# Optimization experiments

Measured on AMD Instinct MI355X. Metric: run time of the kernel, lower is better.

Reference implementation:

```python
import jax, jax.numpy as jnp
import numpy as np

N_NODES = 100000
N_EDGES = 1600000
NFEAT = 256
NHID = 128


def _l2_normalize(v, eps=1e-12):
    return v / (jnp.linalg.norm(v) + eps)


def setup_inputs() -> dict:
    key = jax.random.key(0)
    k1, k2, k3, k4 = jax.random.split(key, 4)
    x = jax.random.normal(k1, (N_NODES, NFEAT), dtype=jnp.float32)
    edge_index = jax.random.randint(k2, (2, N_EDGES), 0, N_NODES, dtype=jnp.int64)
    # GCNConv weight (glorot-ish scale), spectral-normalized at forward time
    W = jax.random.normal(k3, (NFEAT, NHID), dtype=jnp.float32) * 0.05
    bias = jnp.zeros((NHID,), dtype=jnp.float32)
    prelu_a = jnp.full((1,), 0.25, dtype=jnp.float32)  # nn.PReLU default slope
    u = _l2_normalize(jax.random.normal(k4, (NFEAT,), dtype=jnp.float32))
    return {"x": x, "edge_index": edge_index, "W": W, "bias": bias,
            "prelu_a": prelu_a, "u": u}


def reference(x, edge_index, W, bias, prelu_a, u):
    # --- spectral_norm: one power iteration (torch default n_power_iterations=1) ---
    v = _l2_normalize(W.T @ u)          # [NHID]
    u2 = _l2_normalize(W @ v)           # [NFEAT]
    sigma = u2 @ (W @ v)
    W_sn = W / sigma

    # --- GCNConv: linear transform, add self-loops, sym-normalize, scatter-add ---
    xw = x @ W_sn                       # [N, NHID]
    n = x.shape[0]
    loops = jnp.arange(n, dtype=edge_index.dtype)
    row = jnp.concatenate([edge_index[0], loops])  # sources
    col = jnp.concatenate([edge_index[1], loops])  # targets
    ones = jnp.ones(row.shape[0], dtype=x.dtype)
    deg = jax.ops.segment_sum(ones, col, num_segments=n)
    dinv = jnp.where(deg > 0, deg ** -0.5, 0.0)
    norm = dinv[row] * dinv[col]        # [E+N]
    msgs = norm[:, None] * xw[row]      # gather at sources
    out = jax.ops.segment_sum(msgs, col, num_segments=n) + bias

    # --- PReLU ---
    return jnp.where(out > 0, out, prelu_a * out)
```

## Files before the change

### kernel.cpp

```cpp
#include <hip/hip_runtime.h>

#define NFEAT 256
#define NHID  128

#define NBK   391
#define EPB   4096
#define NBLK  391
#define SEGW  4608

typedef __bf16 bf16x8 __attribute__((ext_vector_type(8)));
typedef __bf16 bf16x4 __attribute__((ext_vector_type(4)));
typedef float  f32x4  __attribute__((ext_vector_type(4)));

__global__ __launch_bounds__(256) void sigma_kernel(const float* __restrict__ W,
                                                    const float* __restrict__ u,
                                                    float* __restrict__ scal,
                                                    int* __restrict__ bucket_fill) {
    __shared__ float v[NHID];
    __shared__ float red[256];
    int tid = threadIdx.x;

    if (tid < NBK) bucket_fill[tid] = 0;
    if (tid + 256 < NBK) bucket_fill[tid + 256] = 0;

    float t = 0.f;
    if (tid < NHID) {
        for (int i = 0; i < NFEAT; ++i) t += W[i * NHID + tid] * u[i];
    }
    red[tid] = (tid < NHID) ? t * t : 0.f;
    __syncthreads();
    for (int s = 128; s > 0; s >>= 1) {
        if (tid < s) red[tid] += red[tid + s];
        __syncthreads();
    }
    float nv = sqrtf(red[0]);
    float inv_nv = 1.f / (nv + 1e-12f);
    __syncthreads();
    if (tid < NHID) v[tid] = t * inv_nv;
    __syncthreads();

    float wv = 0.f;
    for (int j = 0; j < NHID; ++j) wv += W[tid * NHID + j] * v[j];
    red[tid] = wv * wv;
    __syncthreads();
    for (int s = 128; s > 0; s >>= 1) {
        if (tid < s) red[tid] += red[tid + s];
        __syncthreads();
    }
    if (tid == 0) {
        float n2  = red[0];
        float nwv = sqrtf(n2);
        float sigma = n2 / (nwv + 1e-12f);
        scal[0] = 1.f / sigma;
    }
}

__global__ __launch_bounds__(256) void wt_kernel(const float* __restrict__ W,
                                                 const float* __restrict__ scal,
                                                 __bf16* __restrict__ WT) {
    int idx = blockIdx.x * 256 + threadIdx.x;
    int c = idx >> 8;
    int r = idx & 255;
    WT[c * NFEAT + r] = (__bf16)(W[r * NHID + c] * scal[0]);
}

__global__ __launch_bounds__(256) void fused_kernel(const float* __restrict__ x,
                                                    const __bf16* __restrict__ WT,
                                                    __bf16* __restrict__ xwb,
                                                    const int* __restrict__ erow,
                                                    const int* __restrict__ ecol,
                                                    int* __restrict__ bucket_fill,
                                                    unsigned int* __restrict__ rbuf,
                                                    int nn, int E, int ngemm) {
    __shared__ __attribute__((aligned(16))) char sbuf[32768];

    int tid  = threadIdx.x;

    if ((int)blockIdx.x < ngemm) {
        float (*xs)[64][64] = (float (*)[64][64])sbuf;

        int lane = tid & 63;
        int w    = tid >> 6;
        int rfrag = lane & 15;
        int kg    = lane >> 4;
        int row0 = blockIdx.x * 64;

        int p16  = lane & 15;
        int rsub = lane >> 4;

        int crow0 = (w & 1) * 32 + rfrag;
        int col0  = (w >> 1) * 64;
        int r0 = row0 + crow0;
        int r1 = r0 + 16;
        const __bf16* wb = WT + (size_t)(col0 + rfrag) * NFEAT + kg * 8;
        int cr7 = crow0 & 7;

        f32x4 acc0[4] = {};
        f32x4 acc1[4] = {};

        auto STAGE = [&](int buf, int c) {
#pragma unroll
            for (int j = 0; j < 4; ++j) {
                int rloc = w * 16 + j * 4 + rsub;
                int grow = row0 + rloc;
                if (grow >= nn) grow = nn - 1;
                const float* src = x + (size_t)grow * NFEAT + c * 64 + ((p16 ^ (grow & 7)) << 2);
                __builtin_amdgcn_global_load_lds(
                    (const __attribute__((address_space(1))) void*)src,
                    (__attribute__((address_space(3))) void*)&xs[buf][w * 16 + j * 4][0],
                    16, 0, 0);
            }
        };

        bf16x8 Bf[2][2][4];
        auto BLOAD = [&](int bbuf, int c) {
#pragma unroll
            for (int ks = 0; ks < 2; ++ks)
#pragma unroll
                for (int nt = 0; nt < 4; ++nt)
                    Bf[bbuf][ks][nt] = *(const bf16x8*)(wb + (size_t)nt * 16 * NFEAT + c * 64 + ks * 32);
        };

        auto MFMA_CHUNK = [&](int buf, int bbuf) {
#pragma unroll
            for (int ks = 0; ks < 2; ++ks) {
                int sA = kg * 2 + ks * 8;
                float4 a0lo = *(const float4*)&xs[buf][crow0][((sA) ^ cr7) * 4];
                float4 a0hi = *(const float4*)&xs[buf][crow0][((sA + 1) ^ cr7) * 4];
                float4 a1lo = *(const float4*)&xs[buf][crow0 + 16][((sA) ^ cr7) * 4];
                float4 a1hi = *(const float4*)&xs[buf][crow0 + 16][((sA + 1) ^ cr7) * 4];
                bf16x8 af0, af1;
                af0[0] = (__bf16)a0lo.x; af0[1] = (__bf16)a0lo.y;
                af0[2] = (__bf16)a0lo.z; af0[3] = (__bf16)a0lo.w;
                af0[4] = (__bf16)a0hi.x; af0[5] = (__bf16)a0hi.y;
                af0[6] = (__bf16)a0hi.z; af0[7] = (__bf16)a0hi.w;
                af1[0] = (__bf16)a1lo.x; af1[1] = (__bf16)a1lo.y;
                af1[2] = (__bf16)a1lo.z; af1[3] = (__bf16)a1lo.w;
                af1[4] = (__bf16)a1hi.x; af1[5] = (__bf16)a1hi.y;
                af1[6] = (__bf16)a1hi.z; af1[7] = (__bf16)a1hi.w;
#pragma unroll
                for (int nt = 0; nt < 4; ++nt) {
                    acc0[nt] = __builtin_amdgcn_mfma_f32_16x16x32_bf16(Bf[bbuf][ks][nt], af0, acc0[nt], 0, 0, 0);
                    acc1[nt] = __builtin_amdgcn_mfma_f32_16x16x32_bf16(Bf[bbuf][ks][nt], af1, acc1[nt], 0, 0, 0);
                }
            }
        };

#define DRAIN_BAR() do { \
            asm volatile("s_waitcnt vmcnt(0)" ::: "memory"); \
            __builtin_amdgcn_s_barrier(); } while (0)

        STAGE(0, 0);
        BLOAD(0, 0);
        DRAIN_BAR();

        BLOAD(1, 1);
        STAGE(1, 1);
        __builtin_amdgcn_sched_barrier(0);
        MFMA_CHUNK(0, 0);
        DRAIN_BAR();

        BLOAD(0, 2);
        STAGE(0, 2);
        __builtin_amdgcn_sched_barrier(0);
        MFMA_CHUNK(1, 1);
        DRAIN_BAR();

        BLOAD(1, 3);
        STAGE(1, 3);
        __builtin_amdgcn_sched_barrier(0);
        MFMA_CHUNK(0, 0);
        DRAIN_BAR();

        MFMA_CHUNK(1, 1);
#undef DRAIN_BAR

        if (r0 < nn) {
            __bf16* orow = xwb + (size_t)r0 * NHID + col0 + kg * 4;
#pragma unroll
            for (int nt = 0; nt < 4; ++nt) {
                bf16x4 v;
                v[0] = (__bf16)acc0[nt][0];
                v[1] = (__bf16)acc0[nt][1];
                v[2] = (__bf16)acc0[nt][2];
                v[3] = (__bf16)acc0[nt][3];
                *(bf16x4*)&orow[nt * 16] = v;
            }
        }
        if (r1 < nn) {
            __bf16* orow = xwb + (size_t)r1 * NHID + col0 + kg * 4;
#pragma unroll
            for (int nt = 0; nt < 4; ++nt) {
                bf16x4 v;
                v[0] = (__bf16)acc1[nt][0];
                v[1] = (__bf16)acc1[nt][1];
                v[2] = (__bf16)acc1[nt][2];
                v[3] = (__bf16)acc1[nt][3];
                *(bf16x4*)&orow[nt * 16] = v;
            }
        }
        return;
    }

    unsigned int*   rec   = (unsigned int*)sbuf;
    unsigned short* bkk   = (unsigned short*)(sbuf + 16384);
    int*            hist  = (int*)(sbuf + 24576);
    int*            lbase = (int*)(sbuf + 24576 + 1564);
    int*            lfill = (int*)(sbuf + 24576 + 3128);
    int*            gb    = (int*)(sbuf + 24576 + 4692);

    int b = blockIdx.x - ngemm;
    for (int k = tid; k < NBK; k += 256) { hist[k] = 0; lfill[k] = 0; }
    __syncthreads();

    int e0 = b * EPB;
    unsigned int rv[16];
    int kv[16];
#pragma unroll
    for (int j = 0; j < 16; ++j) {
        int idx = e0 + j * 256 + tid;
        if (idx < E) {
            int c = ecol[idx];
            int s = erow[idx];
            int k = c >> 8;
            kv[j] = k;
            rv[j] = ((unsigned int)(c & 255) << 24) | (unsigned int)s;
            atomicAdd(&hist[k], 1);
        } else kv[j] = -1;
    }
    __syncthreads();

    if (tid < 64) {
        int carry = 0;
        for (int c0 = 0; c0 < NBK; c0 += 64) {
            int i = c0 + tid;
            int vv = (i < NBK) ? hist[i] : 0;
            int orig = vv;
#pragma unroll
            for (int d = 1; d < 64; d <<= 1) {
                int t = __shfl_up(vv, (unsigned)d, 64);
                if (tid >= d) vv += t;
            }
            if (i < NBK) lbase[i] = carry + vv - orig;
            carry += __shfl(vv, 63, 64);
        }
    }
    __syncthreads();

    if (tid < NBK) gb[tid] = tid * SEGW + atomicAdd(&bucket_fill[tid], hist[tid]);
    if (tid + 256 < NBK) gb[tid + 256] = (tid + 256) * SEGW
                                       + atomicAdd(&bucket_fill[tid + 256], hist[tid + 256]);
    __syncthreads();

#pragma unroll
    for (int j = 0; j < 16; ++j) {
        if (kv[j] >= 0) {
            int p = lbase[kv[j]] + atomicAdd(&lfill[kv[j]], 1);
            rec[p] = rv[j];
            bkk[p] = (unsigned short)kv[j];
        }
    }
    __syncthreads();

    int nval = E - e0;
    if (nval > EPB) nval = EPB;
    for (int p = tid; p < nval; p += 256) {
        int k = bkk[p];
        rbuf[gb[k] + (p - lbase[k])] = rec[p];
    }
}

__global__ __launch_bounds__(256) void fine_kernel(const unsigned int* __restrict__ rbuf,
                                                   const int* __restrict__ bucket_fill,
                                                   int* __restrict__ base_g,
                                                   int* __restrict__ cnt_g,
                                                   float* __restrict__ dinv,
                                                   int* __restrict__ ebuf, int n) {
    __shared__ int cnt[256], lb[256], lf[256], sc[256];
    int tid = threadIdx.x, k = blockIdx.x;
    int seg0 = k * SEGW, seg1 = seg0 + bucket_fill[k];
    cnt[tid] = 0;
    lf[tid] = 0;
    __syncthreads();
    for (int j = seg0 + tid; j < seg1; j += 256)
        atomicAdd(&cnt[rbuf[j] >> 24], 1);
    __syncthreads();
    int cv = cnt[tid];
    sc[tid] = cv;
    __syncthreads();
    int val = cv;
    for (int off = 1; off < 256; off <<= 1) {
        int t = (tid >= off) ? sc[tid - off] : 0;
        __syncthreads();
        val += t;
        sc[tid] = val;
        __syncthreads();
    }
    lb[tid] = val - cv;
    __syncthreads();
    int node = k * 256 + tid;
    if (node < n) {
        base_g[node] = seg0 + lb[tid];
        cnt_g[node] = cv;
        dinv[node] = rsqrtf((float)cv + 1.f);
    }
    for (int j = seg0 + tid; j < seg1; j += 256) {
        unsigned int r = rbuf[j];
        int dl = r >> 24;
        int p = seg0 + lb[dl] + atomicAdd(&lf[dl], 1);
        ebuf[p] = (int)(r & 0xFFFFFFu);
    }
}

__global__ __launch_bounds__(256) void gather_kernel(const uint4* __restrict__ xb4,
                                                     const int* __restrict__ base,
                                                     const int* __restrict__ cnt,
                                                     const int* __restrict__ ebuf,
                                                     const float* __restrict__ dinv,
                                                     const float* __restrict__ bias,
                                                     const float* __restrict__ pa,
                                                     float* __restrict__ out, int n) {
    int tid = threadIdx.x;
    int sub = tid & 15;
    int node = (blockIdx.x * 256 + tid) >> 4;
    if (node >= n) return;

    int b = base[node];
    int deg = cnt[node];
    float dn = dinv[node];

    uint4 s0 = xb4[(size_t)node * 16 + sub];
    float a0 = dn * __uint_as_float(s0.x << 16);
    float a1 = dn * __uint_as_float(s0.x & 0xffff0000u);
    float a2 = dn * __uint_as_float(s0.y << 16);
    float a3 = dn * __uint_as_float(s0.y & 0xffff0000u);
    float a4 = dn * __uint_as_float(s0.z << 16);
    float a5 = dn * __uint_as_float(s0.z & 0xffff0000u);
    float a6 = dn * __uint_as_float(s0.w << 16);
    float a7 = dn * __uint_as_float(s0.w & 0xffff0000u);

    int k = 0;
    for (; k + 4 <= deg; k += 4) {
        int r0 = ebuf[b + k + 0];
        int r1 = ebuf[b + k + 1];
        int r2 = ebuf[b + k + 2];
        int r3 = ebuf[b + k + 3];
        float d0 = dinv[r0], d1 = dinv[r1], d2 = dinv[r2], d3 = dinv[r3];
        uint4 v0 = xb4[(size_t)r0 * 16 + sub];
        uint4 v1 = xb4[(size_t)r1 * 16 + sub];
        uint4 v2 = xb4[(size_t)r2 * 16 + sub];
        uint4 v3 = xb4[(size_t)r3 * 16 + sub];
        a0 += d0 * __uint_as_float(v0.x << 16) + d1 * __uint_as_float(v1.x << 16)
            + d2 * __uint_as_float(v2.x << 16) + d3 * __uint_as_float(v3.x << 16);
        a1 += d0 * __uint_as_float(v0.x & 0xffff0000u) + d1 * __uint_as_float(v1.x & 0xffff0000u)
            + d2 * __uint_as_float(v2.x & 0xffff0000u) + d3 * __uint_as_float(v3.x & 0xffff0000u);
        a2 += d0 * __uint_as_float(v0.y << 16) + d1 * __uint_as_float(v1.y << 16)
            + d2 * __uint_as_float(v2.y << 16) + d3 * __uint_as_float(v3.y << 16);
        a3 += d0 * __uint_as_float(v0.y & 0xffff0000u) + d1 * __uint_as_float(v1.y & 0xffff0000u)
            + d2 * __uint_as_float(v2.y & 0xffff0000u) + d3 * __uint_as_float(v3.y & 0xffff0000u);
        a4 += d0 * __uint_as_float(v0.z << 16) + d1 * __uint_as_float(v1.z << 16)
            + d2 * __uint_as_float(v2.z << 16) + d3 * __uint_as_float(v3.z << 16);
        a5 += d0 * __uint_as_float(v0.z & 0xffff0000u) + d1 * __uint_as_float(v1.z & 0xffff0000u)
            + d2 * __uint_as_float(v2.z & 0xffff0000u) + d3 * __uint_as_float(v3.z & 0xffff0000u);
        a6 += d0 * __uint_as_float(v0.w << 16) + d1 * __uint_as_float(v1.w << 16)
            + d2 * __uint_as_float(v2.w << 16) + d3 * __uint_as_float(v3.w << 16);
        a7 += d0 * __uint_as_float(v0.w & 0xffff0000u) + d1 * __uint_as_float(v1.w & 0xffff0000u)
            + d2 * __uint_as_float(v2.w & 0xffff0000u) + d3 * __uint_as_float(v3.w & 0xffff0000u);
    }
    for (; k < deg; ++k) {
        int r = ebuf[b + k];
        float d = dinv[r];
        uint4 v = xb4[(size_t)r * 16 + sub];
        a0 += d * __uint_as_float(v.x << 16);
        a1 += d * __uint_as_float(v.x & 0xffff0000u);
        a2 += d * __uint_as_float(v.y << 16);
        a3 += d * __uint_as_float(v.y & 0xffff0000u);
        a4 += d * __uint_as_float(v.z << 16);
        a5 += d * __uint_as_float(v.z & 0xffff0000u);
        a6 += d * __uint_as_float(v.w << 16);
        a7 += d * __uint_as_float(v.w & 0xffff0000u);
    }

    float alpha = pa[0];
    const float4* bb4 = (const float4*)bias;
    float4 b0 = bb4[sub * 2], b1 = bb4[sub * 2 + 1];
    float o0 = dn * a0 + b0.x;
    float o1 = dn * a1 + b0.y;
    float o2 = dn * a2 + b0.z;
    float o3 = dn * a3 + b0.w;
    float o4 = dn * a4 + b1.x;
    float o5 = dn * a5 + b1.y;
    float o6 = dn * a6 + b1.z;
    float o7 = dn * a7 + b1.w;
    o0 = o0 > 0.f ? o0 : alpha * o0;
    o1 = o1 > 0.f ? o1 : alpha * o1;
    o2 = o2 > 0.f ? o2 : alpha * o2;
    o3 = o3 > 0.f ? o3 : alpha * o3;
    o4 = o4 > 0.f ? o4 : alpha * o4;
    o5 = o5 > 0.f ? o5 : alpha * o5;
    o6 = o6 > 0.f ? o6 : alpha * o6;
    o7 = o7 > 0.f ? o7 : alpha * o7;
    float4* orow = (float4*)out + (size_t)node * 32 + sub * 2;
    orow[0] = make_float4(o0, o1, o2, o3);
    orow[1] = make_float4(o4, o5, o6, o7);
}

extern "C" void kernel_launch(void* const* d_in, const int* in_sizes, int n_in,
                              void* d_out, int out_size, void* d_ws, size_t ws_size,
                              hipStream_t stream) {
    const float* x    = (const float*)d_in[0];
    const int*   ei   = (const int*)d_in[1];
    const float* W    = (const float*)d_in[2];
    const float* bias = (const float*)d_in[3];
    const float* pa   = (const float*)d_in[4];
    const float* u    = (const float*)d_in[5];

    int n = in_sizes[0] / NFEAT;
    int e = in_sizes[1] / 2;
    const int* erow = ei;
    const int* ecol = ei + e;

    float* out = (float*)d_out;
    char* ws = (char*)d_ws;
    float*        scal   = (float*)(ws);
    int*          bfill  = (int*)  (ws + 0x0002000);
    __bf16*       WT     = (__bf16*)(ws + 0x0010000);
    int*          base_g = (int*)  (ws + 0x0100000);
    int*          cnt_g  = (int*)  (ws + 0x0200000);
    float*        dinv   = (float*)(ws + 0x0300000);
    unsigned int* rbuf   = (unsigned int*)(ws + 0x0500000);
    int*          ebuf   = (int*)  (ws + 0x0C00000);
    __bf16*       xwb    = (__bf16*)(ws + 0x1300000);

    int ngemm = (n + 63) / 64;

    sigma_kernel<<<1, 256, 0, stream>>>(W, u, scal, bfill);
    wt_kernel<<<(NFEAT * NHID) / 256, 256, 0, stream>>>(W, scal, WT);

    fused_kernel<<<ngemm + NBLK, 256, 0, stream>>>(x, WT, xwb, erow, ecol,
                                                   bfill, rbuf, n, e, ngemm);

    fine_kernel<<<NBK, 256, 0, stream>>>(rbuf, bfill, base_g, cnt_g, dinv, ebuf, n);

    long long gunits = (long long)n * 16;
    gather_kernel<<<(int)((gunits + 255) / 256), 256, 0, stream>>>(
        (const uint4*)xwb, base_g, cnt_g, ebuf, dinv, bias, pa, out, n);
}
```

Measured before the change: 146.2 us.

## Split gather feature columns across blocks and pack per-node metadata

The gather kernel now gives each block one 16-column slice of the output for 32 nodes. Consecutive blocks share the same nodes but cover different column slices, so each block's random reads of neighbor rows touch a smaller part of xw, which may improve cache locality. Each thread loads 4 bytes per neighbor instead of 16, which gives more threads and more in-flight loads but narrower accesses, and edge indices and dinv are re-read 8 times. Per-node base, count and dinv are packed into one int4 so they come from a single load.

```diff
diff --git a/kernel.cpp b/kernel.cpp
--- a/kernel.cpp
+++ b/kernel.cpp
@@ -272,8 +272,7 @@
 
 __global__ __launch_bounds__(256) void fine_kernel(const unsigned int* __restrict__ rbuf,
                                                    const int* __restrict__ bucket_fill,
-                                                   int* __restrict__ base_g,
-                                                   int* __restrict__ cnt_g,
+                                                   int4* __restrict__ meta,
                                                    float* __restrict__ dinv,
                                                    int* __restrict__ ebuf, int n) {
     __shared__ int cnt[256], lb[256], lf[256], sc[256];
@@ -300,9 +299,14 @@
     __syncthreads();
     int node = k * 256 + tid;
     if (node < n) {
-        base_g[node] = seg0 + lb[tid];
-        cnt_g[node] = cv;
-        dinv[node] = rsqrtf((float)cv + 1.f);
+        float dv = rsqrtf((float)cv + 1.f);
+        int4 m;
+        m.x = seg0 + lb[tid];
+        m.y = cv;
+        m.z = __float_as_int(dv);
+        m.w = 0;
+        meta[node] = m;
+        dinv[node] = dv;
     }
     for (int j = seg0 + tid; j < seg1; j += 256) {
         unsigned int r = rbuf[j];
@@ -312,32 +316,28 @@
     }
 }
 
-__global__ __launch_bounds__(256) void gather_kernel(const uint4* __restrict__ xb4,
-                                                     const int* __restrict__ base,
-                                                     const int* __restrict__ cnt,
+__global__ __launch_bounds__(256) void gather_kernel(const unsigned int* __restrict__ xbd,
+                                                     const int4* __restrict__ meta,
                                                      const int* __restrict__ ebuf,
                                                      const float* __restrict__ dinv,
                                                      const float* __restrict__ bias,
                                                      const float* __restrict__ pa,
                                                      float* __restrict__ out, int n) {
     int tid = threadIdx.x;
-    int sub = tid & 15;
-    int node = (blockIdx.x * 256 + tid) >> 4;
+    int l = tid & 7;
+    int s = blockIdx.x & 7;
+    int node = (blockIdx.x >> 3) * 32 + (tid >> 3);
     if (node >= n) return;
 
-    int b = base[node];
-    int deg = cnt[node];
-    float dn = dinv[node];
-
-    uint4 s0 = xb4[(size_t)node * 16 + sub];
-    float a0 = dn * __uint_as_float(s0.x << 16);
-    float a1 = dn * __uint_as_float(s0.x & 0xffff0000u);
-    float a2 = dn * __uint_as_float(s0.y << 16);
-    float a3 = dn * __uint_as_float(s0.y & 0xffff0000u);
-    float a4 = dn * __uint_as_float(s0.z << 16);
-    float a5 = dn * __uint_as_float(s0.z & 0xffff0000u);
-    float a6 = dn * __uint_as_float(s0.w << 16);
-    float a7 = dn * __uint_as_float(s0.w & 0xffff0000u);
+    int4 m = meta[node];
+    int b = m.x, deg = m.y;
+    float dn = __int_as_float(m.z);
+    int co = s * 8 + l;
+    const unsigned int* xc = xbd + co;
+
+    unsigned int v = xc[(size_t)node * 64];
+    float a0 = dn * __uint_as_float(v << 16);
+    float a1 = dn * __uint_as_float(v & 0xffff0000u);
 
     int k = 0;
     for (; k + 4 <= deg; k += 4) {
@@ -346,63 +346,30 @@
         int r2 = ebuf[b + k + 2];
         int r3 = ebuf[b + k + 3];
         float d0 = dinv[r0], d1 = dinv[r1], d2 = dinv[r2], d3 = dinv[r3];
-        uint4 v0 = xb4[(size_t)r0 * 16 + sub];
-        uint4 v1 = xb4[(size_t)r1 * 16 + sub];
-        uint4 v2 = xb4[(size_t)r2 * 16 + sub];
-        uint4 v3 = xb4[(size_t)r3 * 16 + sub];
-        a0 += d0 * __uint_as_float(v0.x << 16) + d1 * __uint_as_float(v1.x << 16)
-            + d2 * __uint_as_float(v2.x << 16) + d3 * __uint_as_float(v3.x << 16);
-        a1 += d0 * __uint_as_float(v0.x & 0xffff0000u) + d1 * __uint_as_float(v1.x & 0xffff0000u)
-            + d2 * __uint_as_float(v2.x & 0xffff0000u) + d3 * __uint_as_float(v3.x & 0xffff0000u);
-        a2 += d0 * __uint_as_float(v0.y << 16) + d1 * __uint_as_float(v1.y << 16)
-            + d2 * __uint_as_float(v2.y << 16) + d3 * __uint_as_float(v3.y << 16);
-        a3 += d0 * __uint_as_float(v0.y & 0xffff0000u) + d1 * __uint_as_float(v1.y & 0xffff0000u)
-            + d2 * __uint_as_float(v2.y & 0xffff0000u) + d3 * __uint_as_float(v3.y & 0xffff0000u);
-        a4 += d0 * __uint_as_float(v0.z << 16) + d1 * __uint_as_float(v1.z << 16)
-            + d2 * __uint_as_float(v2.z << 16) + d3 * __uint_as_float(v3.z << 16);
-        a5 += d0 * __uint_as_float(v0.z & 0xffff0000u) + d1 * __uint_as_float(v1.z & 0xffff0000u)
-            + d2 * __uint_as_float(v2.z & 0xffff0000u) + d3 * __uint_as_float(v3.z & 0xffff0000u);
-        a6 += d0 * __uint_as_float(v0.w << 16) + d1 * __uint_as_float(v1.w << 16)
-            + d2 * __uint_as_float(v2.w << 16) + d3 * __uint_as_float(v3.w << 16);
-        a7 += d0 * __uint_as_float(v0.w & 0xffff0000u) + d1 * __uint_as_float(v1.w & 0xffff0000u)
-            + d2 * __uint_as_float(v2.w & 0xffff0000u) + d3 * __uint_as_float(v3.w & 0xffff0000u);
+        unsigned int v0 = xc[(size_t)r0 * 64];
+        unsigned int v1 = xc[(size_t)r1 * 64];
+        unsigned int v2 = xc[(size_t)r2 * 64];
+        unsigned int v3 = xc[(size_t)r3 * 64];
+        a0 += d0 * __uint_as_float(v0 << 16) + d1 * __uint_as_float(v1 << 16)
+            + d2 * __uint_as_float(v2 << 16) + d3 * __uint_as_float(v3 << 16);
+        a1 += d0 * __uint_as_float(v0 & 0xffff0000u) + d1 * __uint_as_float(v1 & 0xffff0000u)
+            + d2 * __uint_as_float(v2 & 0xffff0000u) + d3 * __uint_as_float(v3 & 0xffff0000u);
     }
     for (; k < deg; ++k) {
         int r = ebuf[b + k];
         float d = dinv[r];
-        uint4 v = xb4[(size_t)r * 16 + sub];
-        a0 += d * __uint_as_float(v.x << 16);
-        a1 += d * __uint_as_float(v.x & 0xffff0000u);
-        a2 += d * __uint_as_float(v.y << 16);
-        a3 += d * __uint_as_float(v.y & 0xffff0000u);
-        a4 += d * __uint_as_float(v.z << 16);
-        a5 += d * __uint_as_float(v.z & 0xffff0000u);
-        a6 += d * __uint_as_float(v.w << 16);
-        a7 += d * __uint_as_float(v.w & 0xffff0000u);
+        unsigned int vv = xc[(size_t)r * 64];
+        a0 += d * __uint_as_float(vv << 16);
+        a1 += d * __uint_as_float(vv & 0xffff0000u);
     }
 
     float alpha = pa[0];
-    const float4* bb4 = (const float4*)bias;
-    float4 b0 = bb4[sub * 2], b1 = bb4[sub * 2 + 1];
-    float o0 = dn * a0 + b0.x;
-    float o1 = dn * a1 + b0.y;
-    float o2 = dn * a2 + b0.z;
-    float o3 = dn * a3 + b0.w;
-    float o4 = dn * a4 + b1.x;
-    float o5 = dn * a5 + b1.y;
-    float o6 = dn * a6 + b1.z;
-    float o7 = dn * a7 + b1.w;
+    float2 bb = ((const float2*)bias)[co];
+    float o0 = dn * a0 + bb.x;
+    float o1 = dn * a1 + bb.y;
     o0 = o0 > 0.f ? o0 : alpha * o0;
     o1 = o1 > 0.f ? o1 : alpha * o1;
-    o2 = o2 > 0.f ? o2 : alpha * o2;
-    o3 = o3 > 0.f ? o3 : alpha * o3;
-    o4 = o4 > 0.f ? o4 : alpha * o4;
-    o5 = o5 > 0.f ? o5 : alpha * o5;
-    o6 = o6 > 0.f ? o6 : alpha * o6;
-    o7 = o7 > 0.f ? o7 : alpha * o7;
-    float4* orow = (float4*)out + (size_t)node * 32 + sub * 2;
-    orow[0] = make_float4(o0, o1, o2, o3);
-    orow[1] = make_float4(o4, o5, o6, o7);
+    ((float2*)out)[(size_t)node * 64 + co] = make_float2(o0, o1);
 }
 
 extern "C" void kernel_launch(void* const* d_in, const int* in_sizes, int n_in,
@@ -425,12 +392,11 @@
     float*        scal   = (float*)(ws);
     int*          bfill  = (int*)  (ws + 0x0002000);
     __bf16*       WT     = (__bf16*)(ws + 0x0010000);
-    int*          base_g = (int*)  (ws + 0x0100000);
-    int*          cnt_g  = (int*)  (ws + 0x0200000);
-    float*        dinv   = (float*)(ws + 0x0300000);
-    unsigned int* rbuf   = (unsigned int*)(ws + 0x0500000);
-    int*          ebuf   = (int*)  (ws + 0x0C00000);
-    __bf16*       xwb    = (__bf16*)(ws + 0x1300000);
+    float*        dinv   = (float*)(ws + 0x0100000);
+    int4*         meta   = (int4*) (ws + 0x0200000);
+    unsigned int* rbuf   = (unsigned int*)(ws + 0x0400000);
+    int*          ebuf   = (int*)  (ws + 0x0B00000);
+    __bf16*       xwb    = (__bf16*)(ws + 0x1200000);
 
     int ngemm = (n + 63) / 64;
 
@@ -440,9 +406,9 @@
     fused_kernel<<<ngemm + NBLK, 256, 0, stream>>>(x, WT, xwb, erow, ecol,
                                                    bfill, rbuf, n, e, ngemm);
 
-    fine_kernel<<<NBK, 256, 0, stream>>>(rbuf, bfill, base_g, cnt_g, dinv, ebuf, n);
-
-    long long gunits = (long long)n * 16;
-    gather_kernel<<<(int)((gunits + 255) / 256), 256, 0, stream>>>(
-        (const uint4*)xwb, base_g, cnt_g, ebuf, dinv, bias, pa, out, n);
-}
+    fine_kernel<<<NBK, 256, 0, stream>>>(rbuf, bfill, meta, dinv, ebuf, n);
+
+    int ngroups = (n + 31) / 32;
+    gather_kernel<<<ngroups * 8, 256, 0, stream>>>(
+        (const unsigned int*)xwb, meta, ebuf, dinv, bias, pa, out, n);
+}
```

New measurement: 285.3 us. 1.95x slower.

## Triple-buffer GEMM x staging with partial vmcnt waits; pack node metadata

Applied to the files above, without the earlier changes.

The GEMM part of the fused kernel now stages x tiles into three LDS buffers (shared memory grows to 48KB). It waits with partial vmcnt counts instead of draining all loads before each barrier, so the next tile's global loads stay in flight during MFMA compute. Separately, per-node base, count and dinv are packed into one int4 record, so the gather kernel does a single 16-byte load per node instead of three scalar loads. The larger LDS footprint may lower occupancy, and the hand-tuned vmcnt values depend on the exact number of loads issued by each stage.

```diff
diff --git a/kernel.cpp b/kernel.cpp
--- a/kernel.cpp
+++ b/kernel.cpp
@@ -11,6 +11,8 @@
 typedef __bf16 bf16x8 __attribute__((ext_vector_type(8)));
 typedef __bf16 bf16x4 __attribute__((ext_vector_type(4)));
 typedef float  f32x4  __attribute__((ext_vector_type(4)));
+
+#define PIN() __builtin_amdgcn_sched_barrier(0)
 
 __global__ __launch_bounds__(256) void sigma_kernel(const float* __restrict__ W,
                                                     const float* __restrict__ u,
@@ -72,7 +74,7 @@
                                                     int* __restrict__ bucket_fill,
                                                     unsigned int* __restrict__ rbuf,
                                                     int nn, int E, int ngemm) {
-    __shared__ __attribute__((aligned(16))) char sbuf[32768];
+    __shared__ __attribute__((aligned(16))) char sbuf[49152];
 
     int tid  = threadIdx.x;
 
@@ -146,34 +148,30 @@
             }
         };
 
-#define DRAIN_BAR() do { \
-            asm volatile("s_waitcnt vmcnt(0)" ::: "memory"); \
-            __builtin_amdgcn_s_barrier(); } while (0)
-
-        STAGE(0, 0);
-        BLOAD(0, 0);
-        DRAIN_BAR();
-
-        BLOAD(1, 1);
-        STAGE(1, 1);
-        __builtin_amdgcn_sched_barrier(0);
+        STAGE(0, 0);  PIN();
+        BLOAD(0, 0);  PIN();
+        STAGE(1, 1);  PIN();
+        asm volatile("s_waitcnt vmcnt(12)" ::: "memory");
+        __builtin_amdgcn_s_barrier();
+
+        BLOAD(1, 1);  PIN();
+        STAGE(2, 2);  PIN();
         MFMA_CHUNK(0, 0);
-        DRAIN_BAR();
-
-        BLOAD(0, 2);
-        STAGE(0, 2);
-        __builtin_amdgcn_sched_barrier(0);
+        asm volatile("s_waitcnt vmcnt(12)" ::: "memory");
+        __builtin_amdgcn_s_barrier();
+
+        BLOAD(0, 2);  PIN();
+        STAGE(0, 3);  PIN();
         MFMA_CHUNK(1, 1);
-        DRAIN_BAR();
-
-        BLOAD(1, 3);
-        STAGE(1, 3);
-        __builtin_amdgcn_sched_barrier(0);
-        MFMA_CHUNK(0, 0);
-        DRAIN_BAR();
-
-        MFMA_CHUNK(1, 1);
-#undef DRAIN_BAR
+        asm volatile("s_waitcnt vmcnt(12)" ::: "memory");
+        __builtin_amdgcn_s_barrier();
+
+        BLOAD(1, 3);  PIN();
+        MFMA_CHUNK(2, 0);
+        asm volatile("s_waitcnt vmcnt(8)" ::: "memory");
+        __builtin_amdgcn_s_barrier();
+
+        MFMA_CHUNK(0, 1);
 
         if (r0 < nn) {
             __bf16* orow = xwb + (size_t)r0 * NHID + col0 + kg * 4;
@@ -272,8 +270,7 @@
 
 __global__ __launch_bounds__(256) void fine_kernel(const unsigned int* __restrict__ rbuf,
                                                    const int* __restrict__ bucket_fill,
-                                                   int* __restrict__ base_g,
-                                                   int* __restrict__ cnt_g,
+                                                   int4* __restrict__ meta,
                                                    float* __restrict__ dinv,
                                                    int* __restrict__ ebuf, int n) {
     __shared__ int cnt[256], lb[256], lf[256], sc[256];
@@ -300,9 +297,14 @@
     __syncthreads();
     int node = k * 256 + tid;
     if (node < n) {
-        base_g[node] = seg0 + lb[tid];
-        cnt_g[node] = cv;
-        dinv[node] = rsqrtf((float)cv + 1.f);
+        float dv = rsqrtf((float)cv + 1.f);
+        int4 m;
+        m.x = seg0 + lb[tid];
+        m.y = cv;
+        m.z = __float_as_int(dv);
+        m.w = 0;
+        meta[node] = m;
+        dinv[node] = dv;
     }
     for (int j = seg0 + tid; j < seg1; j += 256) {
         unsigned int r = rbuf[j];
@@ -313,8 +315,7 @@
 }
 
 __global__ __launch_bounds__(256) void gather_kernel(const uint4* __restrict__ xb4,
-                                                     const int* __restrict__ base,
-                                                     const int* __restrict__ cnt,
+                                                     const int4* __restrict__ meta,
                                                      const int* __restrict__ ebuf,
                                                      const float* __restrict__ dinv,
                                                      const float* __restrict__ bias,
@@ -325,9 +326,9 @@
     int node = (blockIdx.x * 256 + tid) >> 4;
     if (node >= n) return;
 
-    int b = base[node];
-    int deg = cnt[node];
-    float dn = dinv[node];
+    int4 m = meta[node];
+    int b = m.x, deg = m.y;
+    float dn = __int_as_float(m.z);
 
     uint4 s0 = xb4[(size_t)node * 16 + sub];
     float a0 = dn * __uint_as_float(s0.x << 16);
@@ -425,12 +426,11 @@
     float*        scal   = (float*)(ws);
     int*          bfill  = (int*)  (ws + 0x0002000);
     __bf16*       WT     = (__bf16*)(ws + 0x0010000);
-    int*          base_g = (int*)  (ws + 0x0100000);
-    int*          cnt_g  = (int*)  (ws + 0x0200000);
-    float*        dinv   = (float*)(ws + 0x0300000);
-    unsigned int* rbuf   = (unsigned int*)(ws + 0x0500000);
-    int*          ebuf   = (int*)  (ws + 0x0C00000);
-    __bf16*       xwb    = (__bf16*)(ws + 0x1300000);
+    float*        dinv   = (float*)(ws + 0x0100000);
+    int4*         meta   = (int4*) (ws + 0x0200000);
+    unsigned int* rbuf   = (unsigned int*)(ws + 0x0400000);
+    int*          ebuf   = (int*)  (ws + 0x0B00000);
+    __bf16*       xwb    = (__bf16*)(ws + 0x1200000);
 
     int ngemm = (n + 63) / 64;
 
@@ -440,9 +440,9 @@
     fused_kernel<<<ngemm + NBLK, 256, 0, stream>>>(x, WT, xwb, erow, ecol,
                                                    bfill, rbuf, n, e, ngemm);
 
-    fine_kernel<<<NBK, 256, 0, stream>>>(rbuf, bfill, base_g, cnt_g, dinv, ebuf, n);
+    fine_kernel<<<NBK, 256, 0, stream>>>(rbuf, bfill, meta, dinv, ebuf, n);
 
     long long gunits = (long long)n * 16;
     gather_kernel<<<(int)((gunits + 255) / 256), 256, 0, stream>>>(
-        (const uint4*)xwb, base_g, cnt_g, ebuf, dinv, bias, pa, out, n);
-}
+        (const uint4*)xwb, meta, ebuf, dinv, bias, pa, out, n);
+}
```

After: 145.5 us. About the same (-0.5%).
